# Kernel optimization log

Measured on AMD Instinct MI355X. Metric: run time of the kernel, lower is better.

## Reference

```python
import jax, jax.numpy as jnp
import numpy as np

N_TOTAL = 1_048_576   # total points across all clouds
B = 4096              # number of point clouds
IN_FEATURES = 4
POINT_DIMS = [4, 64, 128, 256, 256]   # point encoding: 3 Linear+LeakyReLU, then final Linear(256,256)
LATENT_DIMS = [256, 256, 256]         # latent encoding: 2 Linear+LeakyReLU
LATENT_DIM = 256


def _linear_params(key, fan_in, fan_out):
    # torch nn.Linear default init: U(-1/sqrt(fan_in), 1/sqrt(fan_in))
    k1, k2 = jax.random.split(key)
    lim = 1.0 / np.sqrt(fan_in)
    w = jax.random.uniform(k1, (fan_out, fan_in), minval=-lim, maxval=lim, dtype=jnp.float32)
    b = jax.random.uniform(k2, (fan_out,), minval=-lim, maxval=lim, dtype=jnp.float32)
    return w, b


def setup_inputs() -> dict:
    key = jax.random.key(0)
    keys = jax.random.split(key, 16)
    inp = {}
    inp["points"] = jax.random.normal(keys[0], (N_TOTAL, IN_FEATURES), dtype=jnp.float32)
    # cumulative segment ends; even partition so no segment is empty (avg 256 pts/cloud)
    inp["idx"] = (jnp.arange(1, B + 1, dtype=jnp.int32) * N_TOTAL) // B
    # point encoding params
    inp["pw0"], inp["pb0"] = _linear_params(keys[1], POINT_DIMS[0], POINT_DIMS[1])
    inp["pw1"], inp["pb1"] = _linear_params(keys[2], POINT_DIMS[1], POINT_DIMS[2])
    inp["pw2"], inp["pb2"] = _linear_params(keys[3], POINT_DIMS[2], POINT_DIMS[3])
    inp["pw3"], inp["pb3"] = _linear_params(keys[4], POINT_DIMS[3], POINT_DIMS[4])
    # latent encoding params
    inp["lw0"], inp["lb0"] = _linear_params(keys[5], LATENT_DIMS[0], LATENT_DIMS[1])
    inp["lw1"], inp["lb1"] = _linear_params(keys[6], LATENT_DIMS[1], LATENT_DIMS[2])
    # mu / logvar heads
    inp["mw"], inp["mb"] = _linear_params(keys[7], LATENT_DIMS[2], LATENT_DIM)
    inp["vw"], inp["vb"] = _linear_params(keys[8], LATENT_DIMS[2], LATENT_DIM)
    return inp


def reference(points, idx, pw0, pb0, pw1, pb1, pw2, pb2, pw3, pb3,
              lw0, lb0, lw1, lb1, mw, mb, vw, vb):
    lrelu = jax.nn.leaky_relu  # default negative_slope=0.01, same as torch LeakyReLU
    h = lrelu(points @ pw0.T + pb0)
    h = lrelu(h @ pw1.T + pb1)
    h = lrelu(h @ pw2.T + pb2)
    h = h @ pw3.T + pb3                          # [N, 256]
    n = h.shape[0]
    b = idx.shape[0]
    # segment id of each point: i s.t. idx[i-1] <= j < idx[i]
    seg = jnp.searchsorted(idx, jnp.arange(n, dtype=idx.dtype), side="right")
    sums = jax.ops.segment_sum(h, seg, num_segments=b)            # [B, 256]
    counts = idx - jnp.concatenate([jnp.zeros((1,), idx.dtype), idx[:-1]])
    latent = sums / counts[:, None].astype(h.dtype)               # per-cloud mean
    # latent encoding
    latent = lrelu(latent @ lw0.T + lb0)
    latent = lrelu(latent @ lw1.T + lb1)
    mu = latent @ mw.T + mb
    log_var = latent @ vw.T + vb
    return mu, log_var
```

## Files before the change

### kernel.cpp

```cpp
#include <hip/hip_runtime.h>


#define NB    4096
#define NTOT  1048576
#define PTS   64
#define OUT_HALF (NB * 256)
#define WSPLIT_ELEMS 106496

typedef __attribute__((ext_vector_type(8))) short short8;
typedef __attribute__((ext_vector_type(4))) float f32x4;
typedef unsigned short u16;
typedef unsigned int   u32;

__device__ __forceinline__ float lrelu(float x){ return x > 0.0f ? x : 0.01f * x; }

__device__ __forceinline__ u16 f2bf(float x){
  union{float f; u32 u;} v; v.f = x;
  u32 r = v.u + 0x7fffu + ((v.u >> 16) & 1u);
  return (u16)(r >> 16);
}
__device__ __forceinline__ float bf2f(u16 h){
  union{u32 u; float f;} v; v.u = ((u32)h) << 16; return v.f;
}

__device__ __forceinline__ int find_cloud(const int* __restrict__ idx, int j){
  int lo = 0, hi = NB;
  while (lo < hi){
    int mid = (lo + hi) >> 1;
    if (idx[mid] <= j) lo = mid + 1; else hi = mid;
  }
  return lo;
}

__global__ void wsplit_kernel(const float* __restrict__ w1,
                              const float* __restrict__ w2,
                              const float* __restrict__ w3,
                              u16* __restrict__ Whi, u16* __restrict__ Wlo){
  const int tid = blockIdx.x * 256 + threadIdx.x;
  const float* W; int K, off;
  if (tid < 8192)       { W = w1; K = 64;  off = 0; }
  else if (tid < 40960) { W = w2; K = 128; off = 8192; }
  else                  { W = w3; K = 256; off = 40960; }
  const int t      = tid - off;
  const int fragId = t >> 9;
  const int r      = t & 511;
  const int lane   = r >> 3, e = r & 7;
  const int KS     = K / 32;
  const int ks     = fragId % KS, mtg = fragId / KS;
  const int m      = mtg * 16 + (lane & 15);
  const int k      = ks * 32 + (lane >> 4) * 8 + e;
  const float v = W[(size_t)m * K + k];
  const u16 hi = f2bf(v);
  const u16 lo = f2bf(v - bf2f(hi));
  Whi[tid] = hi; Wlo[tid] = lo;
}

template<int K, int M, int LDSKI, int LDSKO, bool WRITE>
__device__ __forceinline__ void mfma_layer(
    const u16* __restrict__ hin, u16* __restrict__ hout,
    const u16* __restrict__ Whi, const u16* __restrict__ Wlo,
    const float* __restrict__ bias, int w, int lane, f32x4 (*__restrict__ accRet)[4])
{
  constexpr int KS  = K / 32;
  constexpr int MTW = M / 64;
  const int lrow = lane & 15;
  const int g    = lane >> 4;

  f32x4 acc[4][MTW];
  #pragma unroll
  for (int mt = 0; mt < MTW; ++mt){
    const float bv = bias[(w * MTW + mt) * 16 + lrow];
    #pragma unroll
    for (int a = 0; a < 4; ++a){
      acc[a][mt][0] = bv; acc[a][mt][1] = bv; acc[a][mt][2] = bv; acc[a][mt][3] = bv;
    }
  }
  #pragma unroll
  for (int ks = 0; ks < KS; ++ks){
    const int eoff = ks * 32 + g * 8;
    short8 af[4];
    #pragma unroll
    for (int a = 0; a < 4; ++a)
      af[a] = *reinterpret_cast<const short8*>(hin + (a * 16 + lrow) * LDSKI + eoff);
    #pragma unroll
    for (int mt = 0; mt < MTW; ++mt){
      const int fragId = (w * MTW + mt) * KS + ks;
      const short8 bh = *reinterpret_cast<const short8*>(Whi + fragId * 512 + lane * 8);
      const short8 bl = *reinterpret_cast<const short8*>(Wlo + fragId * 512 + lane * 8);
      #pragma unroll
      for (int a = 0; a < 4; ++a)
        acc[a][mt] = __builtin_amdgcn_mfma_f32_16x16x32_bf16(af[a], bh, acc[a][mt], 0, 0, 0);
      #pragma unroll
      for (int a = 0; a < 4; ++a)
        acc[a][mt] = __builtin_amdgcn_mfma_f32_16x16x32_bf16(af[a], bl, acc[a][mt], 0, 0, 0);
    }
  }
  if constexpr (WRITE){
    #pragma unroll
    for (int a = 0; a < 4; ++a)
      #pragma unroll
      for (int mt = 0; mt < MTW; ++mt){
        const int m = (w * MTW + mt) * 16 + lrow;
        #pragma unroll
        for (int r = 0; r < 4; ++r){
          const int pt = a * 16 + g * 4 + r;
          hout[pt * LDSKO + m] = f2bf(lrelu(acc[a][mt][r]));
        }
      }
  } else {
    #pragma unroll
    for (int a = 0; a < 4; ++a)
      #pragma unroll
      for (int mt = 0; mt < MTW; ++mt)
        accRet[a][mt] = acc[a][mt];
  }
}

__global__ __launch_bounds__(256, 2)
void point_mfma_kernel(const float* __restrict__ points, const int* __restrict__ idx,
    const float* __restrict__ w0, const float* __restrict__ b0,
    const float* __restrict__ b1, const float* __restrict__ b2,
    const float* __restrict__ b3,
    const u16* __restrict__ Whi, const u16* __restrict__ Wlo,
    float* __restrict__ sums)
{
  __shared__ u16 h1[PTS][72];
  __shared__ u16 h2[PTS][136];
  __shared__ u16 h3[PTS][264];

  const int t    = threadIdx.x;
  const int base = blockIdx.x * PTS;
  const int w    = t >> 6;
  const int lane = t & 63;

  {
    const int pt  = t & 63;
    const int grp = t >> 6;
    const float4 pv = *reinterpret_cast<const float4*>(points + (size_t)(base + pt) * 4);
    #pragma unroll
    for (int j = 0; j < 16; ++j){
      const int m = grp * 16 + j;
      const float4 wv = *reinterpret_cast<const float4*>(w0 + m * 4);
      const float s = b0[m] + pv.x * wv.x + pv.y * wv.y + pv.z * wv.z + pv.w * wv.w;
      h1[pt][m] = f2bf(lrelu(s));
    }
  }
  __syncthreads();
  mfma_layer< 64, 128,  72, 136, true >(&h1[0][0], &h2[0][0], Whi + 0,     Wlo + 0,     b1, w, lane, nullptr);
  __syncthreads();
  mfma_layer<128, 256, 136, 264, true >(&h2[0][0], &h3[0][0], Whi + 8192,  Wlo + 8192,  b2, w, lane, nullptr);
  __syncthreads();
  f32x4 acc3[4][4];
  mfma_layer<256, 256, 264,   1, false>(&h3[0][0], nullptr,   Whi + 40960, Wlo + 40960, b3, w, lane, acc3);

  const int lrow = lane & 15;
  const int cF = find_cloud(idx, base);
  const int cL = find_cloud(idx, base + PTS - 1);
  if (cF == cL){
    #pragma unroll
    for (int mt = 0; mt < 4; ++mt){
      float s = 0.0f;
      #pragma unroll
      for (int a = 0; a < 4; ++a){
        const f32x4 v = acc3[a][mt];
        s += v[0] + v[1] + v[2] + v[3];
      }
      s += __shfl_xor(s, 16, 64);
      s += __shfl_xor(s, 32, 64);
      if (lane < 16)
        atomicAdd(sums + (size_t)cF * 256 + (w * 4 + mt) * 16 + lrow, s);
    }
  } else {
    const int g = lane >> 4;
    #pragma unroll
    for (int a = 0; a < 4; ++a)
      #pragma unroll
      for (int mt = 0; mt < 4; ++mt)
        #pragma unroll
        for (int r = 0; r < 4; ++r){
          const int pt = base + a * 16 + g * 4 + r;
          const int c  = find_cloud(idx, pt);
          atomicAdd(sums + (size_t)c * 256 + (w * 4 + mt) * 16 + lrow, acc3[a][mt][r]);
        }
  }
}

__device__ __forceinline__ void lat_accum(const float (*__restrict__ in)[256],
    const float* __restrict__ W, const float* __restrict__ bias, int t, float acc[4])
{
  const float bv = bias[t];
  #pragma unroll
  for (int cl = 0; cl < 4; ++cl) acc[cl] = bv;
  const float4* __restrict__ wrow = reinterpret_cast<const float4*>(W + (size_t)t * 256);
  #pragma unroll 4
  for (int k4 = 0; k4 < 64; ++k4){
    const float4 w = wrow[k4];
    #pragma unroll
    for (int cl = 0; cl < 4; ++cl){
      const float4 a = *reinterpret_cast<const float4*>(&in[cl][k4 * 4]);
      acc[cl] += a.x * w.x + a.y * w.y + a.z * w.z + a.w * w.w;
    }
  }
}

__global__ __launch_bounds__(256)
void latent_kernel(const float* __restrict__ sums, const int* __restrict__ idx,
    const float* __restrict__ lw0, const float* __restrict__ lb0,
    const float* __restrict__ lw1, const float* __restrict__ lb1,
    const float* __restrict__ mw, const float* __restrict__ mb,
    const float* __restrict__ vw, const float* __restrict__ vb,
    float* __restrict__ out)
{
  __shared__ float s_in[4][256];
  __shared__ float s_a[4][256];
  const int t  = threadIdx.x;
  const int c0 = blockIdx.x * 4;

  #pragma unroll
  for (int cl = 0; cl < 4; ++cl){
    const int c = c0 + cl;
    const int cnt = idx[c] - (c ? idx[c - 1] : 0);
    s_in[cl][t] = sums[(size_t)c * 256 + t] / (float)cnt;
  }
  __syncthreads();

  float acc[4];
  lat_accum(s_in, lw0, lb0, t, acc);
  #pragma unroll
  for (int cl = 0; cl < 4; ++cl) s_a[cl][t] = lrelu(acc[cl]);
  __syncthreads();

  lat_accum(s_a, lw1, lb1, t, acc);
  __syncthreads();
  #pragma unroll
  for (int cl = 0; cl < 4; ++cl) s_in[cl][t] = lrelu(acc[cl]);
  __syncthreads();

  float accm[4], accv[4];
  lat_accum(s_in, mw, mb, t, accm);
  lat_accum(s_in, vw, vb, t, accv);
  #pragma unroll
  for (int cl = 0; cl < 4; ++cl){
    out[(size_t)(c0 + cl) * 256 + t]                    = accm[cl];
    out[(size_t)OUT_HALF + (size_t)(c0 + cl) * 256 + t] = accv[cl];
  }
}

extern "C" void kernel_launch(void* const* d_in, const int* in_sizes, int n_in,
                              void* d_out, int out_size, void* d_ws, size_t ws_size,
                              hipStream_t stream) {
  const float* points = (const float*)d_in[0];
  const int*   idx    = (const int*)  d_in[1];
  const float* pw0 = (const float*)d_in[2],  *pb0 = (const float*)d_in[3];
  const float* pw1 = (const float*)d_in[4],  *pb1 = (const float*)d_in[5];
  const float* pw2 = (const float*)d_in[6],  *pb2 = (const float*)d_in[7];
  const float* pw3 = (const float*)d_in[8],  *pb3 = (const float*)d_in[9];
  const float* lw0 = (const float*)d_in[10], *lb0 = (const float*)d_in[11];
  const float* lw1 = (const float*)d_in[12], *lb1 = (const float*)d_in[13];
  const float* mw  = (const float*)d_in[14], *mb  = (const float*)d_in[15];
  const float* vw  = (const float*)d_in[16], *vb  = (const float*)d_in[17];
  float* out  = (float*)d_out;

  const size_t sums_bytes = (size_t)NB * 256 * sizeof(float);
  const size_t wsplit_bytes = (size_t)WSPLIT_ELEMS * 2;
  float* sums; u16* Whi; u16* Wlo;
  if (ws_size >= sums_bytes + 2 * wsplit_bytes){
    sums = (float*)d_ws;
    Whi  = (u16*)((char*)d_ws + sums_bytes);
    Wlo  = Whi + WSPLIT_ELEMS;
  } else {
    Whi  = (u16*)d_out;
    Wlo  = Whi + WSPLIT_ELEMS;
    sums = out + OUT_HALF;
  }

  hipMemsetAsync(sums, 0, sums_bytes, stream);
  wsplit_kernel<<<WSPLIT_ELEMS / 256, 256, 0, stream>>>(pw1, pw2, pw3, Whi, Wlo);
  point_mfma_kernel<<<NTOT / PTS, 256, 0, stream>>>(points, idx,
      pw0, pb0, pb1, pb2, pb3, Whi, Wlo, sums);
  latent_kernel<<<NB / 4, 256, 0, stream>>>(sums, idx,
      lw0, lb0, lw1, lb1, mw, mb, vw, vb, out);
}
```

Before: 1.166 ms.

## Double-buffer MFMA operand loads, alias LDS buffers, raise occupancy target

Software-pipelines the MFMA layer loop by prefetching the next k-step's LDS activation fragments and global weight fragments while the current step's MFMAs run. It also overlays the h1 and h3 LDS buffers in one shared allocation (h1 is dead once h3 is written), which cuts LDS per block so that three blocks per CU can fit. The launch bound rises from 2 to 3 blocks per CU. The prefetch adds register pressure, which with the tighter occupancy bound may cause spills, and the aliasing relies on correct barrier ordering between layers.

```diff
diff --git a/kernel.cpp b/kernel.cpp
--- a/kernel.cpp
+++ b/kernel.cpp
@@ -75,26 +75,51 @@
       acc[a][mt][0] = bv; acc[a][mt][1] = bv; acc[a][mt][2] = bv; acc[a][mt][3] = bv;
     }
   }
+
+  const u16* __restrict__ bptr = Whi + (size_t)(w * MTW) * KS * 512 + lane * 8;
+  const u16* __restrict__ lptr = Wlo + (size_t)(w * MTW) * KS * 512 + lane * 8;
+
+  short8 af[4], bh[MTW], bl[MTW];
+  #pragma unroll
+  for (int a = 0; a < 4; ++a)
+    af[a] = *reinterpret_cast<const short8*>(hin + (a * 16 + lrow) * LDSKI + g * 8);
+  #pragma unroll
+  for (int mt = 0; mt < MTW; ++mt){
+    bh[mt] = *reinterpret_cast<const short8*>(bptr + (size_t)mt * KS * 512);
+    bl[mt] = *reinterpret_cast<const short8*>(lptr + (size_t)mt * KS * 512);
+  }
+
   #pragma unroll
   for (int ks = 0; ks < KS; ++ks){
-    const int eoff = ks * 32 + g * 8;
-    short8 af[4];
-    #pragma unroll
-    for (int a = 0; a < 4; ++a)
-      af[a] = *reinterpret_cast<const short8*>(hin + (a * 16 + lrow) * LDSKI + eoff);
+    short8 af2[4], bh2[MTW], bl2[MTW];
+    if (ks + 1 < KS){
+      const int eoff2 = (ks + 1) * 32 + g * 8;
+      #pragma unroll
+      for (int a = 0; a < 4; ++a)
+        af2[a] = *reinterpret_cast<const short8*>(hin + (a * 16 + lrow) * LDSKI + eoff2);
+      #pragma unroll
+      for (int mt = 0; mt < MTW; ++mt){
+        bh2[mt] = *reinterpret_cast<const short8*>(bptr + (size_t)(mt * KS + ks + 1) * 512);
+        bl2[mt] = *reinterpret_cast<const short8*>(lptr + (size_t)(mt * KS + ks + 1) * 512);
+      }
+    }
     #pragma unroll
     for (int mt = 0; mt < MTW; ++mt){
-      const int fragId = (w * MTW + mt) * KS + ks;
-      const short8 bh = *reinterpret_cast<const short8*>(Whi + fragId * 512 + lane * 8);
-      const short8 bl = *reinterpret_cast<const short8*>(Wlo + fragId * 512 + lane * 8);
       #pragma unroll
       for (int a = 0; a < 4; ++a)
-        acc[a][mt] = __builtin_amdgcn_mfma_f32_16x16x32_bf16(af[a], bh, acc[a][mt], 0, 0, 0);
+        acc[a][mt] = __builtin_amdgcn_mfma_f32_16x16x32_bf16(af[a], bh[mt], acc[a][mt], 0, 0, 0);
       #pragma unroll
       for (int a = 0; a < 4; ++a)
-        acc[a][mt] = __builtin_amdgcn_mfma_f32_16x16x32_bf16(af[a], bl, acc[a][mt], 0, 0, 0);
-    }
-  }
+        acc[a][mt] = __builtin_amdgcn_mfma_f32_16x16x32_bf16(af[a], bl[mt], acc[a][mt], 0, 0, 0);
+    }
+    if (ks + 1 < KS){
+      #pragma unroll
+      for (int a = 0; a < 4; ++a) af[a] = af2[a];
+      #pragma unroll
+      for (int mt = 0; mt < MTW; ++mt){ bh[mt] = bh2[mt]; bl[mt] = bl2[mt]; }
+    }
+  }
+
   if constexpr (WRITE){
     #pragma unroll
     for (int a = 0; a < 4; ++a)
@@ -116,7 +141,7 @@
   }
 }
 
-__global__ __launch_bounds__(256, 2)
+__global__ __launch_bounds__(256, 3)
 void point_mfma_kernel(const float* __restrict__ points, const int* __restrict__ idx,
     const float* __restrict__ w0, const float* __restrict__ b0,
     const float* __restrict__ b1, const float* __restrict__ b2,
@@ -124,9 +149,10 @@
     const u16* __restrict__ Whi, const u16* __restrict__ Wlo,
     float* __restrict__ sums)
 {
-  __shared__ u16 h1[PTS][72];
-  __shared__ u16 h2[PTS][136];
-  __shared__ u16 h3[PTS][264];
+  __shared__ __align__(16) char smem[51200];
+  u16 (*h2)[136] = reinterpret_cast<u16(*)[136]>(smem);
+  u16 (*h1)[72]  = reinterpret_cast<u16(*)[72]>(smem + 17408);
+  u16 (*h3)[264] = reinterpret_cast<u16(*)[264]>(smem + 17408);
 
   const int t    = threadIdx.x;
   const int base = blockIdx.x * PTS;
```

Result: faster. 965.1 us (-17.2%).

## Stream weight chunks into LDS with double-buffered async loads and swizzled activations

Applied to the files above, without the earlier changes.

Weights are repacked into 52 chunks of hi and lo bf16 fragments. Each chunk is copied asynchronously from global memory into a double-buffered LDS area with global_load_lds while the previous chunk feeds the MFMAs, so B-operand fragments no longer come from per-wave global loads. Activation buffers now use an XOR swizzle instead of padding, h2 and h3 share memory, and launch bounds are raised to 3 blocks per CU. The latent kernel handles 16 clouds per block instead of 4, which cuts weight re-reads. The cost is a barrier after every chunk and more registers per thread in the latent kernel.

```diff
diff --git a/kernel.cpp b/kernel.cpp
--- a/kernel.cpp
+++ b/kernel.cpp
@@ -5,12 +5,16 @@
 #define NTOT  1048576
 #define PTS   64
 #define OUT_HALF (NB * 256)
-#define WSPLIT_ELEMS 106496
+#define NCHUNK 52
+#define CHUNK_U16 4096
+#define WSTG_ELEMS (NCHUNK * CHUNK_U16)
 
 typedef __attribute__((ext_vector_type(8))) short short8;
 typedef __attribute__((ext_vector_type(4))) float f32x4;
 typedef unsigned short u16;
 typedef unsigned int   u32;
+typedef __attribute__((address_space(1))) u32 gu32;
+typedef __attribute__((address_space(3))) u32 lu32;
 
 __device__ __forceinline__ float lrelu(float x){ return x > 0.0f ? x : 0.01f * x; }
 
@@ -35,37 +39,41 @@
 __global__ void wsplit_kernel(const float* __restrict__ w1,
                               const float* __restrict__ w2,
                               const float* __restrict__ w3,
-                              u16* __restrict__ Whi, u16* __restrict__ Wlo){
+                              u16* __restrict__ Wstg){
   const int tid = blockIdx.x * 256 + threadIdx.x;
-  const float* W; int K, off;
-  if (tid < 8192)       { W = w1; K = 64;  off = 0; }
-  else if (tid < 40960) { W = w2; K = 128; off = 8192; }
-  else                  { W = w3; K = 256; off = 40960; }
-  const int t      = tid - off;
-  const int fragId = t >> 9;
-  const int r      = t & 511;
-  const int lane   = r >> 3, e = r & 7;
-  const int KS     = K / 32;
-  const int ks     = fragId % KS, mtg = fragId / KS;
-  const int m      = mtg * 16 + (lane & 15);
-  const int k      = ks * 32 + (lane >> 4) * 8 + e;
+  const int g = tid >> 12;
+  const int r = tid & 4095;
+  const float* W; int K, MTW, ks, mt;
+  if (g < 4)      { W = w1; K = 64;  MTW = 2; ks = g >> 1;  mt = g & 1; }
+  else if (g < 20){ int cc = g - 4;  W = w2; K = 128; MTW = 4; ks = cc >> 2; mt = cc & 3; }
+  else            { int cc = g - 20; W = w3; K = 256; MTW = 4; ks = cc >> 2; mt = cc & 3; }
+  const int w    = r >> 10;
+  const int rem  = r & 1023;
+  const int hl   = rem >> 9;
+  const int fe   = rem & 511;
+  const int lane = fe >> 3, e = fe & 7;
+  const int m = (w * MTW + mt) * 16 + (lane & 15);
+  const int k = ks * 32 + (lane >> 4) * 8 + e;
   const float v = W[(size_t)m * K + k];
   const u16 hi = f2bf(v);
-  const u16 lo = f2bf(v - bf2f(hi));
-  Whi[tid] = hi; Wlo[tid] = lo;
-}
-
-template<int K, int M, int LDSKI, int LDSKO, bool WRITE>
-__device__ __forceinline__ void mfma_layer(
-    const u16* __restrict__ hin, u16* __restrict__ hout,
-    const u16* __restrict__ Whi, const u16* __restrict__ Wlo,
-    const float* __restrict__ bias, int w, int lane, f32x4 (*__restrict__ accRet)[4])
+  Wstg[tid] = hl ? f2bf(v - bf2f(hi)) : hi;
+}
+
+__device__ __forceinline__ void stage_chunk(const u16* __restrict__ Wstg,
+                                            char* wbuf, int gc, int t){
+  const u16* src = Wstg + ((size_t)gc << 12) + t * 8;
+  char* dst = wbuf + ((gc & 1) << 13) + t * 16;
+  __builtin_amdgcn_global_load_lds((const gu32*)(src),        (lu32*)(dst),        16, 0, 0);
+  __builtin_amdgcn_global_load_lds((const gu32*)(src + 2048), (lu32*)(dst + 4096), 16, 0, 0);
+}
+
+template<int K, int M, int RBI, int RBO, int GBASE, bool WRITE, bool PRE_BAR>
+__device__ __forceinline__ void layer_run(
+    const char* hin, char* hout, const u16* __restrict__ Wstg, char* wbuf,
+    const float* __restrict__ bias, int w, int lane, int t, f32x4 (*accRet)[4])
 {
-  constexpr int KS  = K / 32;
-  constexpr int MTW = M / 64;
-  const int lrow = lane & 15;
-  const int g    = lane >> 4;
-
+  constexpr int KS = K / 32, MTW = M / 64, NCH = KS * MTW;
+  const int lrow = lane & 15, g = lane >> 4;
   f32x4 acc[4][MTW];
   #pragma unroll
   for (int mt = 0; mt < MTW; ++mt){
@@ -75,64 +83,78 @@
       acc[a][mt][0] = bv; acc[a][mt][1] = bv; acc[a][mt][2] = bv; acc[a][mt][3] = bv;
     }
   }
-  #pragma unroll
-  for (int ks = 0; ks < KS; ++ks){
-    const int eoff = ks * 32 + g * 8;
-    short8 af[4];
+  short8 af[4];
+  #pragma unroll
+  for (int c = 0; c < NCH; ++c){
+    const int gc = GBASE + c;
+    if (gc + 1 < NCHUNK) stage_chunk(Wstg, wbuf, gc + 1, t);
+    const int ks = c / MTW, mt = c % MTW;
+    if (mt == 0){
+      const int ko = ks * 64 + g * 16;
+      #pragma unroll
+      for (int a = 0; a < 4; ++a){
+        const int pt = a * 16 + lrow;
+        af[a] = *reinterpret_cast<const short8*>(hin + pt * RBI + (ko ^ ((pt & 7) << 4)));
+      }
+    }
+    const char* wb = wbuf + ((gc & 1) << 13) + (w << 11) + (lane << 4);
+    const short8 bh = *reinterpret_cast<const short8*>(wb);
+    const short8 bl = *reinterpret_cast<const short8*>(wb + 1024);
     #pragma unroll
     for (int a = 0; a < 4; ++a)
-      af[a] = *reinterpret_cast<const short8*>(hin + (a * 16 + lrow) * LDSKI + eoff);
-    #pragma unroll
-    for (int mt = 0; mt < MTW; ++mt){
-      const int fragId = (w * MTW + mt) * KS + ks;
-      const short8 bh = *reinterpret_cast<const short8*>(Whi + fragId * 512 + lane * 8);
-      const short8 bl = *reinterpret_cast<const short8*>(Wlo + fragId * 512 + lane * 8);
-      #pragma unroll
-      for (int a = 0; a < 4; ++a)
-        acc[a][mt] = __builtin_amdgcn_mfma_f32_16x16x32_bf16(af[a], bh, acc[a][mt], 0, 0, 0);
-      #pragma unroll
-      for (int a = 0; a < 4; ++a)
-        acc[a][mt] = __builtin_amdgcn_mfma_f32_16x16x32_bf16(af[a], bl, acc[a][mt], 0, 0, 0);
-    }
-  }
-  if constexpr (WRITE){
+      acc[a][mt] = __builtin_amdgcn_mfma_f32_16x16x32_bf16(af[a], bh, acc[a][mt], 0, 0, 0);
+    #pragma unroll
+    for (int a = 0; a < 4; ++a)
+      acc[a][mt] = __builtin_amdgcn_mfma_f32_16x16x32_bf16(af[a], bl, acc[a][mt], 0, 0, 0);
+    if (c == NCH - 1){
+      if constexpr (PRE_BAR) __syncthreads();
+      if constexpr (WRITE){
+        #pragma unroll
+        for (int a = 0; a < 4; ++a)
+          #pragma unroll
+          for (int mt2 = 0; mt2 < MTW; ++mt2){
+            const int m = (w * MTW + mt2) * 16 + lrow;
+            #pragma unroll
+            for (int r2 = 0; r2 < 4; ++r2){
+              const int pt = a * 16 + g * 4 + r2;
+              *reinterpret_cast<u16*>(hout + pt * RBO + ((m * 2) ^ ((pt & 7) << 4)))
+                  = f2bf(lrelu(acc[a][mt2][r2]));
+            }
+          }
+      }
+    }
+    __syncthreads();
+  }
+  if constexpr (!WRITE){
     #pragma unroll
     for (int a = 0; a < 4; ++a)
       #pragma unroll
-      for (int mt = 0; mt < MTW; ++mt){
-        const int m = (w * MTW + mt) * 16 + lrow;
-        #pragma unroll
-        for (int r = 0; r < 4; ++r){
-          const int pt = a * 16 + g * 4 + r;
-          hout[pt * LDSKO + m] = f2bf(lrelu(acc[a][mt][r]));
-        }
-      }
-  } else {
-    #pragma unroll
-    for (int a = 0; a < 4; ++a)
-      #pragma unroll
-      for (int mt = 0; mt < MTW; ++mt)
-        accRet[a][mt] = acc[a][mt];
-  }
-}
-
-__global__ __launch_bounds__(256, 2)
+      for (int mt2 = 0; mt2 < MTW; ++mt2)
+        accRet[a][mt2] = acc[a][mt2];
+  }
+}
+
+__global__ __launch_bounds__(256, 3)
 void point_mfma_kernel(const float* __restrict__ points, const int* __restrict__ idx,
     const float* __restrict__ w0, const float* __restrict__ b0,
     const float* __restrict__ b1, const float* __restrict__ b2,
     const float* __restrict__ b3,
-    const u16* __restrict__ Whi, const u16* __restrict__ Wlo,
+    const u16* __restrict__ Wstg,
     float* __restrict__ sums)
 {
-  __shared__ u16 h1[PTS][72];
-  __shared__ u16 h2[PTS][136];
-  __shared__ u16 h3[PTS][264];
+  __shared__ __align__(16) char smem[49152];
+  char* h3   = smem;
+  char* h2   = smem;
+  char* h1   = smem + 16384;
+  char* wbuf = smem + 32768;
 
   const int t    = threadIdx.x;
   const int base = blockIdx.x * PTS;
   const int w    = t >> 6;
   const int lane = t & 63;
 
+  stage_chunk(Wstg, wbuf, 0, t);
+
   {
     const int pt  = t & 63;
     const int grp = t >> 6;
@@ -142,16 +164,15 @@
       const int m = grp * 16 + j;
       const float4 wv = *reinterpret_cast<const float4*>(w0 + m * 4);
       const float s = b0[m] + pv.x * wv.x + pv.y * wv.y + pv.z * wv.z + pv.w * wv.w;
-      h1[pt][m] = f2bf(lrelu(s));
-    }
-  }
-  __syncthreads();
-  mfma_layer< 64, 128,  72, 136, true >(&h1[0][0], &h2[0][0], Whi + 0,     Wlo + 0,     b1, w, lane, nullptr);
-  __syncthreads();
-  mfma_layer<128, 256, 136, 264, true >(&h2[0][0], &h3[0][0], Whi + 8192,  Wlo + 8192,  b2, w, lane, nullptr);
-  __syncthreads();
+      *reinterpret_cast<u16*>(h1 + pt * 128 + ((m * 2) ^ ((pt & 7) << 4))) = f2bf(lrelu(s));
+    }
+  }
+  __syncthreads();
+
+  layer_run< 64, 128, 128, 256,  0, true,  false>(h1, h2, Wstg, wbuf, b1, w, lane, t, nullptr);
+  layer_run<128, 256, 256, 512,  4, true,  true >(h2, h3, Wstg, wbuf, b2, w, lane, t, nullptr);
   f32x4 acc3[4][4];
-  mfma_layer<256, 256, 264,   1, false>(&h3[0][0], nullptr,   Whi + 40960, Wlo + 40960, b3, w, lane, acc3);
+  layer_run<256, 256, 512,   1, 20, false, false>(h3, nullptr, Wstg, wbuf, b3, w, lane, t, acc3);
 
   const int lrow = lane & 15;
   const int cF = find_cloud(idx, base);
@@ -185,18 +206,19 @@
   }
 }
 
+#define CPB 16
 __device__ __forceinline__ void lat_accum(const float (*__restrict__ in)[256],
-    const float* __restrict__ W, const float* __restrict__ bias, int t, float acc[4])
+    const float* __restrict__ W, const float* __restrict__ bias, int t, float* acc)
 {
   const float bv = bias[t];
   #pragma unroll
-  for (int cl = 0; cl < 4; ++cl) acc[cl] = bv;
+  for (int cl = 0; cl < CPB; ++cl) acc[cl] = bv;
   const float4* __restrict__ wrow = reinterpret_cast<const float4*>(W + (size_t)t * 256);
   #pragma unroll 4
   for (int k4 = 0; k4 < 64; ++k4){
     const float4 w = wrow[k4];
     #pragma unroll
-    for (int cl = 0; cl < 4; ++cl){
+    for (int cl = 0; cl < CPB; ++cl){
       const float4 a = *reinterpret_cast<const float4*>(&in[cl][k4 * 4]);
       acc[cl] += a.x * w.x + a.y * w.y + a.z * w.z + a.w * w.w;
     }
@@ -211,36 +233,36 @@
     const float* __restrict__ vw, const float* __restrict__ vb,
     float* __restrict__ out)
 {
-  __shared__ float s_in[4][256];
-  __shared__ float s_a[4][256];
+  __shared__ float s_in[CPB][256];
+  __shared__ float s_a[CPB][256];
   const int t  = threadIdx.x;
-  const int c0 = blockIdx.x * 4;
-
-  #pragma unroll
-  for (int cl = 0; cl < 4; ++cl){
+  const int c0 = blockIdx.x * CPB;
+
+  #pragma unroll
+  for (int cl = 0; cl < CPB; ++cl){
     const int c = c0 + cl;
     const int cnt = idx[c] - (c ? idx[c - 1] : 0);
     s_in[cl][t] = sums[(size_t)c * 256 + t] / (float)cnt;
   }
   __syncthreads();
 
-  float acc[4];
+  float acc[CPB];
   lat_accum(s_in, lw0, lb0, t, acc);
   #pragma unroll
-  for (int cl = 0; cl < 4; ++cl) s_a[cl][t] = lrelu(acc[cl]);
+  for (int cl = 0; cl < CPB; ++cl) s_a[cl][t] = lrelu(acc[cl]);
   __syncthreads();
 
   lat_accum(s_a, lw1, lb1, t, acc);
   __syncthreads();
   #pragma unroll
-  for (int cl = 0; cl < 4; ++cl) s_in[cl][t] = lrelu(acc[cl]);
-  __syncthreads();
-
-  float accm[4], accv[4];
+  for (int cl = 0; cl < CPB; ++cl) s_in[cl][t] = lrelu(acc[cl]);
+  __syncthreads();
+
+  float accm[CPB], accv[CPB];
   lat_accum(s_in, mw, mb, t, accm);
   lat_accum(s_in, vw, vb, t, accv);
   #pragma unroll
-  for (int cl = 0; cl < 4; ++cl){
+  for (int cl = 0; cl < CPB; ++cl){
     out[(size_t)(c0 + cl) * 256 + t]                    = accm[cl];
     out[(size_t)OUT_HALF + (size_t)(c0 + cl) * 256 + t] = accv[cl];
   }
@@ -262,22 +284,20 @@
   float* out  = (float*)d_out;
 
   const size_t sums_bytes = (size_t)NB * 256 * sizeof(float);
-  const size_t wsplit_bytes = (size_t)WSPLIT_ELEMS * 2;
-  float* sums; u16* Whi; u16* Wlo;
-  if (ws_size >= sums_bytes + 2 * wsplit_bytes){
+  const size_t wstg_bytes = (size_t)WSTG_ELEMS * 2;
+  float* sums; u16* Wstg;
+  if (ws_size >= sums_bytes + wstg_bytes){
     sums = (float*)d_ws;
-    Whi  = (u16*)((char*)d_ws + sums_bytes);
-    Wlo  = Whi + WSPLIT_ELEMS;
+    Wstg = (u16*)((char*)d_ws + sums_bytes);
   } else {
-    Whi  = (u16*)d_out;
-    Wlo  = Whi + WSPLIT_ELEMS;
+    Wstg = (u16*)d_out;
     sums = out + OUT_HALF;
   }
 
   hipMemsetAsync(sums, 0, sums_bytes, stream);
-  wsplit_kernel<<<WSPLIT_ELEMS / 256, 256, 0, stream>>>(pw1, pw2, pw3, Whi, Wlo);
+  wsplit_kernel<<<WSTG_ELEMS / 256, 256, 0, stream>>>(pw1, pw2, pw3, Wstg);
   point_mfma_kernel<<<NTOT / PTS, 256, 0, stream>>>(points, idx,
-      pw0, pb0, pb1, pb2, pb3, Whi, Wlo, sums);
-  latent_kernel<<<NB / 4, 256, 0, stream>>>(sums, idx,
+      pw0, pb0, pb1, pb2, pb3, Wstg, sums);
+  latent_kernel<<<NB / CPB, 256, 0, stream>>>(sums, idx,
       lw0, lb0, lw1, lb1, mw, mb, vw, vb, out);
 }
```

After: 1.098 ms. -5.9%, faster.
